# Optimization experiments

Measured on AMD Instinct MI355X. Metric: run time of the kernel, lower is better.

The kernel has to match this reference:

```python
import jax, jax.numpy as jnp
import numpy as np

N = 8192
IN, HID, NH, TOT = 64, 64, 4, 128
DH = TOT // NH  # 32


def setup_inputs() -> dict:
    key = jax.random.key(0)
    ks = jax.random.split(key, 8)
    s = 0.05
    return {
        "input": jax.random.normal(ks[0], (N, IN), jnp.float32),
        "hx": jax.random.normal(ks[1], (N, HID), jnp.float32),
        "Wq": jax.random.normal(ks[2], (NH, TOT, DH), jnp.float32) * s,
        "Wk": jax.random.normal(ks[3], (NH, TOT, DH), jnp.float32) * s,
        "Wr": jax.random.normal(ks[4], (TOT, HID), jnp.float32) * s,
        "br": jnp.zeros((HID,), jnp.float32),
        "Wz": jax.random.normal(ks[5], (TOT, HID), jnp.float32) * s,
        "bz": jnp.zeros((HID,), jnp.float32),
        "Wh": jax.random.normal(ks[6], (TOT, HID), jnp.float32) * s,
        "bh": jnp.zeros((HID,), jnp.float32),
    }


def _dyn_adj(x, Wq, Wk):
    # x: [N, T]; multi-head attention adjacency, averaged over heads -> [N, N]
    q = jnp.einsum('nt,htd->hnd', x, Wq)
    k = jnp.einsum('nt,htd->hnd', x, Wk)
    scores = jnp.einsum('hnd,hmd->hnm', q, k) / jnp.sqrt(jnp.float32(DH))
    return jnp.mean(jax.nn.softmax(scores, axis=-1), axis=0)  # [N, N]


def reference(input, hx, Wq, Wk, Wr, br, Wz, bz, Wh, bh):
    x = jnp.concatenate([input, hx], axis=1)          # [N, TOT]
    adj = _dyn_adj(x, Wq, Wk)                         # [N, N] row-stochastic
    ax = adj @ x                                      # shared adjacency application
    r = jax.nn.sigmoid(ax @ Wr + br)                  # [N, HID]
    z = jax.nn.sigmoid(ax @ Wz + bz)                  # [N, HID]
    x2 = jnp.concatenate([input, r * hx], axis=1)     # [N, TOT]
    h = jnp.tanh((adj @ x2) @ Wh + bh)                # [N, HID]
    return z * hx + (1.0 - z) * h
```

## Files before the change

kernel.cpp:

```cpp
#include <hip/hip_runtime.h>
#include <hip/hip_bf16.h>

#define NN 8192
#define TOTD 128
#define HIDD 64
#define NHEAD 4
#define DHD 32
#define NCQ 16
#define JPB (NN / 32 / NCQ)

typedef __attribute__((ext_vector_type(8))) short short8;
typedef __attribute__((ext_vector_type(4))) float f32x4;

__device__ __forceinline__ short f2b(float f) {
  unsigned u = __builtin_bit_cast(unsigned, f);
  u += 0x7fff + ((u >> 16) & 1);
  return (short)(u >> 16);
}
__device__ __forceinline__ short f2b_fast(float f) {
  unsigned u = __builtin_bit_cast(unsigned, f);
  return (short)((u + 0x8000u) >> 16);
}
__device__ __forceinline__ float fexp2(float x) {
#if __has_builtin(__builtin_amdgcn_exp2f)
  return __builtin_amdgcn_exp2f(x);
#else
  return exp2f(x);
#endif
}

__device__ __forceinline__ void gl_lds16(const short* g, short* l) {
  __builtin_amdgcn_global_load_lds(
      (const __attribute__((address_space(1))) void*)g,
      (__attribute__((address_space(3))) void*)l, 16, 0, 0);
}

__global__ void k_build_xfrag(const float* __restrict__ in, const float* __restrict__ hx,
                              short* __restrict__ xb) {
  int i = blockIdx.x * 256 + threadIdx.x;
  int n = i >> 7;
  int t = i & 127;
  float v = (t < 64) ? in[n * 64 + t] : hx[n * 64 + (t - 64)];
  int jt = n >> 5, kk = n & 31, cg = t >> 4;
  int l = ((kk >> 3) << 4) | (t & 15);
  xb[(((size_t)jt * 8 + cg) << 9) + (l << 3) + (kk & 7)] = f2b(v);
}

__global__ void k_qk(const float* __restrict__ in, const float* __restrict__ hx,
                     const float* __restrict__ Wq, const float* __restrict__ Wk,
                     short* __restrict__ qb, short* __restrict__ kb) {
  __shared__ float xr[TOTD];
  int n = blockIdx.x;
  int tid = threadIdx.x;
  if (tid < TOTD) xr[tid] = (tid < 64) ? in[n * 64 + tid] : hx[n * 64 + (tid - 64)];
  __syncthreads();
  int which = tid >> 7;
  int h = (tid >> 5) & 3;
  int d = tid & 31;
  const float* W = (which ? Wk : Wq) + h * TOTD * DHD + d;
  float acc = 0.f;
#pragma unroll
  for (int t = 0; t < TOTD; ++t) acc += xr[t] * W[t * DHD];
  int l = ((d >> 3) << 4) | (n & 15);
  if (!which) {
    acc *= 0.25503486f;
    qb[(((size_t)(n >> 4) * 4 + h) << 9) + (l << 3) + (d & 7)] = f2b(acc);
  } else {
    kb[((((size_t)(n >> 5) * 4 + h) * 2 + ((n >> 4) & 1)) << 9) + (l << 3) + (d & 7)] = f2b(acc);
  }
}

__global__ __launch_bounds__(256, 8) void k_denom(
    const short* __restrict__ qb, const short* __restrict__ kb,
    float* __restrict__ lpart_g) {
  __shared__ short kbuf[8 * 512];
  const int tid = threadIdx.x;
  const int w = tid >> 6, l = tid & 63;
  const int row16 = l & 15, grp = l >> 4;
  const int r0 = blockIdx.x * 64 + w * 16;
  const int rtile = blockIdx.x * 4 + w;
  const int jt0 = blockIdx.y * JPB;
  const f32x4 zero4 = {0.f, 0.f, 0.f, 0.f};

  short8 qf[NHEAD];
#pragma unroll
  for (int h = 0; h < NHEAD; ++h)
    qf[h] = *(const short8*)&qb[(((size_t)rtile * 4 + h) << 9) + l * 8];

  float acc[NHEAD][4];
#pragma unroll
  for (int h = 0; h < NHEAD; ++h)
#pragma unroll
    for (int r = 0; r < 4; ++r) acc[h][r] = 0.f;

  for (int j = 0; j < JPB; ++j) {
    int jt = jt0 + j;
#pragma unroll
    for (int c = w * 2; c < w * 2 + 2; ++c)
      gl_lds16(kb + (((size_t)jt * 8 + c) << 9) + l * 8, &kbuf[c * 512]);
    __syncthreads();
#pragma unroll
    for (int hs = 0; hs < 8; ++hs) {
      short8 kf = *(const short8*)&kbuf[hs * 512 + l * 8];
      f32x4 s = __builtin_amdgcn_mfma_f32_16x16x32_bf16(qf[hs >> 1], kf, zero4, 0, 0, 0);
#pragma unroll
      for (int r = 0; r < 4; ++r) acc[hs >> 1][r] += fexp2(s[r]);
    }
    __syncthreads();
  }
#pragma unroll
  for (int m = 1; m < 16; m <<= 1)
#pragma unroll
    for (int h = 0; h < NHEAD; ++h)
#pragma unroll
      for (int r = 0; r < 4; ++r) acc[h][r] += __shfl_xor(acc[h][r], m, 64);

  if (row16 == 0) {
#pragma unroll
    for (int h = 0; h < NHEAD; ++h)
#pragma unroll
      for (int r = 0; r < 4; ++r)
        lpart_g[((size_t)blockIdx.y * NHEAD + h) * NN + r0 + grp * 4 + r] = acc[h][r];
  }
}

__global__ void k_linv(const float* __restrict__ lpart_g, float* __restrict__ linv_g) {
  int i = blockIdx.x * 256 + threadIdx.x;
  float s = 0.f;
#pragma unroll
  for (int q = 0; q < NCQ; ++q) s += lpart_g[(size_t)q * NHEAD * NN + i];
  linv_g[i] = 0.25f / s;
}

__global__ __launch_bounds__(256, 5) void k_pv1(
    const short* __restrict__ qb, const short* __restrict__ kb,
    const short* __restrict__ xb, const float* __restrict__ linv_g,
    float* __restrict__ axq) {
  __shared__ short kxbuf[16 * 512];
  __shared__ short Plds[4][16][40];
  const int tid = threadIdx.x;
  const int w = tid >> 6, l = tid & 63;
  const int row16 = l & 15, grp = l >> 4;
  const int r0 = blockIdx.x * 64 + w * 16;
  const int rtile = blockIdx.x * 4 + w;
  const int jt0 = blockIdx.y * JPB;
  const f32x4 zero4 = {0.f, 0.f, 0.f, 0.f};

  short8 qf[NHEAD];
#pragma unroll
  for (int h = 0; h < NHEAD; ++h)
    qf[h] = *(const short8*)&qb[(((size_t)rtile * 4 + h) << 9) + l * 8];
  float linv[NHEAD][4];
#pragma unroll
  for (int h = 0; h < NHEAD; ++h)
#pragma unroll
    for (int r = 0; r < 4; ++r) linv[h][r] = linv_g[h * NN + r0 + grp * 4 + r];

  f32x4 axa[8];
#pragma unroll
  for (int cg = 0; cg < 8; ++cg) axa[cg] = zero4;

  for (int j = 0; j < JPB; ++j) {
    int jt = jt0 + j;
#pragma unroll
    for (int c = w * 4; c < w * 4 + 4; ++c) {
      const short* src = (c < 8) ? kb + (((size_t)jt * 8 + c) << 9) + l * 8
                                 : xb + (((size_t)jt * 8 + (c - 8)) << 9) + l * 8;
      gl_lds16(src, &kxbuf[c * 512]);
    }
    __syncthreads();
#pragma unroll
    for (int sub = 0; sub < 2; ++sub) {
      float p[4] = {0.f, 0.f, 0.f, 0.f};
#pragma unroll
      for (int h = 0; h < NHEAD; ++h) {
        short8 kf = *(const short8*)&kxbuf[(h * 2 + sub) * 512 + l * 8];
        f32x4 s = __builtin_amdgcn_mfma_f32_16x16x32_bf16(qf[h], kf, zero4, 0, 0, 0);
#pragma unroll
        for (int r = 0; r < 4; ++r) p[r] += fexp2(s[r]) * linv[h][r];
      }
#pragma unroll
      for (int r = 0; r < 4; ++r)
        Plds[w][grp * 4 + r][sub * 16 + row16] = f2b_fast(p[r]);
    }
    short8 pa = *(short8*)&Plds[w][row16][grp * 8];
#pragma unroll
    for (int cg = 0; cg < 8; ++cg) {
      short8 xv = *(const short8*)&kxbuf[(8 + cg) * 512 + l * 8];
      axa[cg] = __builtin_amdgcn_mfma_f32_16x16x32_bf16(pa, xv, axa[cg], 0, 0, 0);
    }
    __syncthreads();
  }
#pragma unroll
  for (int cg = 0; cg < 8; ++cg)
#pragma unroll
    for (int r = 0; r < 4; ++r)
      axq[(size_t)blockIdx.y * NN * TOTD + (size_t)(r0 + grp * 4 + r) * TOTD + cg * 16 + row16] =
          axa[cg][r];
}

__global__ void k_rz(const float* __restrict__ axq, const float* __restrict__ hx,
                     const float* __restrict__ Wr, const float* __restrict__ br,
                     const float* __restrict__ Wz, const float* __restrict__ bz,
                     float* __restrict__ ax, float* __restrict__ z,
                     short* __restrict__ v2f) {
  __shared__ float axs[2][TOTD];
  int tid = threadIdx.x;
  int rr = tid >> 7;
  int c2 = tid & 127;
  int n = blockIdx.x * 2 + rr;
  float s = 0.f;
#pragma unroll
  for (int q = 0; q < NCQ; ++q) s += axq[(size_t)q * NN * TOTD + (size_t)n * TOTD + c2];
  axs[rr][c2] = s;
  ax[(size_t)n * TOTD + c2] = s;
  __syncthreads();
  bool isz = c2 >= HIDD;
  int c = c2 & (HIDD - 1);
  const float* W = isz ? Wz : Wr;
  float acc = isz ? bz[c] : br[c];
#pragma unroll
  for (int t = 0; t < TOTD; ++t) acc += axs[rr][t] * W[t * HIDD + c];
  float sg = 1.f / (1.f + __expf(-acc));
  if (isz) {
    z[n * HIDD + c] = sg;
  } else {
    int jt = n >> 5, kk = n & 31, cg = c >> 4;
    int ll = ((kk >> 3) << 4) | (c & 15);
    v2f[(((size_t)jt * 4 + cg) << 9) + (ll << 3) + (kk & 7)] = f2b(sg * hx[n * HIDD + c]);
  }
}

__global__ __launch_bounds__(256, 5) void k_pv2(
    const short* __restrict__ qb, const short* __restrict__ kb,
    const short* __restrict__ v2f, const float* __restrict__ linv_g,
    float* __restrict__ a2q) {
  __shared__ short kvbuf[12 * 512];
  __shared__ short Plds[4][16][40];
  const int tid = threadIdx.x;
  const int w = tid >> 6, l = tid & 63;
  const int row16 = l & 15, grp = l >> 4;
  const int r0 = blockIdx.x * 64 + w * 16;
  const int rtile = blockIdx.x * 4 + w;
  const int jt0 = blockIdx.y * JPB;
  const f32x4 zero4 = {0.f, 0.f, 0.f, 0.f};

  short8 qf[NHEAD];
#pragma unroll
  for (int h = 0; h < NHEAD; ++h)
    qf[h] = *(const short8*)&qb[(((size_t)rtile * 4 + h) << 9) + l * 8];
  float linv[NHEAD][4];
#pragma unroll
  for (int h = 0; h < NHEAD; ++h)
#pragma unroll
    for (int r = 0; r < 4; ++r) linv[h][r] = linv_g[h * NN + r0 + grp * 4 + r];

  f32x4 a2a[4];
#pragma unroll
  for (int cg = 0; cg < 4; ++cg) a2a[cg] = zero4;

  for (int j = 0; j < JPB; ++j) {
    int jt = jt0 + j;
#pragma unroll
    for (int c = w * 3; c < w * 3 + 3; ++c) {
      const short* src = (c < 8) ? kb + (((size_t)jt * 8 + c) << 9) + l * 8
                                 : v2f + (((size_t)jt * 4 + (c - 8)) << 9) + l * 8;
      gl_lds16(src, &kvbuf[c * 512]);
    }
    __syncthreads();
#pragma unroll
    for (int sub = 0; sub < 2; ++sub) {
      float p[4] = {0.f, 0.f, 0.f, 0.f};
#pragma unroll
      for (int h = 0; h < NHEAD; ++h) {
        short8 kf = *(const short8*)&kvbuf[(h * 2 + sub) * 512 + l * 8];
        f32x4 s = __builtin_amdgcn_mfma_f32_16x16x32_bf16(qf[h], kf, zero4, 0, 0, 0);
#pragma unroll
        for (int r = 0; r < 4; ++r) p[r] += fexp2(s[r]) * linv[h][r];
      }
#pragma unroll
      for (int r = 0; r < 4; ++r)
        Plds[w][grp * 4 + r][sub * 16 + row16] = f2b_fast(p[r]);
    }
    short8 pa = *(short8*)&Plds[w][row16][grp * 8];
#pragma unroll
    for (int cg = 0; cg < 4; ++cg) {
      short8 vv = *(const short8*)&kvbuf[(8 + cg) * 512 + l * 8];
      a2a[cg] = __builtin_amdgcn_mfma_f32_16x16x32_bf16(pa, vv, a2a[cg], 0, 0, 0);
    }
    __syncthreads();
  }
#pragma unroll
  for (int cg = 0; cg < 4; ++cg)
#pragma unroll
    for (int r = 0; r < 4; ++r)
      a2q[(size_t)blockIdx.y * NN * HIDD + (size_t)(r0 + grp * 4 + r) * HIDD + cg * 16 + row16] =
          a2a[cg][r];
}

__global__ __launch_bounds__(256) void k_final(
    const float* __restrict__ a2q, const float* __restrict__ ax,
    const float* __restrict__ hx, const float* __restrict__ Wh,
    const float* __restrict__ bh, const float* __restrict__ z,
    float* __restrict__ out) {
  __shared__ float Whs[TOTD * HIDD];
  __shared__ float a2s[16][HIDD];
  const int tid = threadIdx.x;
  const int r0 = blockIdx.x * 16;

  for (int i = tid; i < TOTD * HIDD; i += 256) Whs[i] = Wh[i];
  for (int i = tid; i < 16 * HIDD; i += 256) {
    int rw = i >> 6, c = i & 63;
    size_t gi = (size_t)(r0 + rw) * HIDD + c;
    float s = 0.f;
#pragma unroll
    for (int q = 0; q < NCQ; ++q) s += a2q[(size_t)q * NN * HIDD + gi];
    a2s[rw][c] = s;
  }
  __syncthreads();
  for (int o = tid; o < 16 * HIDD; o += 256) {
    int rw = o >> 6, c = o & 63;
    const float* axrow = &ax[(size_t)(r0 + rw) * TOTD];
    float acc = bh[c];
#pragma unroll
    for (int t = 0; t < 64; ++t) acc += axrow[t] * Whs[t * HIDD + c];
#pragma unroll
    for (int t = 0; t < 64; ++t) acc += a2s[rw][t] * Whs[(64 + t) * HIDD + c];
    float hval = tanhf(acc);
    size_t gi = (size_t)(r0 + rw) * HIDD + c;
    float zz = z[gi];
    out[gi] = zz * hx[gi] + (1.f - zz) * hval;
  }
}

extern "C" void kernel_launch(void* const* d_in, const int* in_sizes, int n_in,
                              void* d_out, int out_size, void* d_ws, size_t ws_size,
                              hipStream_t stream) {
  const float* in = (const float*)d_in[0];
  const float* hx = (const float*)d_in[1];
  const float* Wq = (const float*)d_in[2];
  const float* Wk = (const float*)d_in[3];
  const float* Wr = (const float*)d_in[4];
  const float* br = (const float*)d_in[5];
  const float* Wz = (const float*)d_in[6];
  const float* bz = (const float*)d_in[7];
  const float* Wh = (const float*)d_in[8];
  const float* bh = (const float*)d_in[9];

  const size_t MB = 1ull << 20;
  char* ws = (char*)d_ws;
  short* qb    = (short*)(ws + 0 * MB);
  short* kb    = (short*)(ws + 2 * MB);
  short* xb    = (short*)(ws + 4 * MB);
  float* linv  = (float*)(ws + 6 * MB);
  float* lpart = (float*)(ws + 7 * MB);
  float* ax    = (float*)(ws + 10 * MB);
  float* z     = (float*)(ws + 14 * MB);
  short* v2f   = (short*)(ws + 16 * MB);
  float* axq   = (float*)(ws + 20 * MB);
  float* a2q   = (float*)(ws + 84 * MB);
  float* out   = (float*)d_out;

  k_build_xfrag<<<dim3((NN * TOTD) / 256), dim3(256), 0, stream>>>(in, hx, xb);
  k_qk<<<dim3(NN), dim3(256), 0, stream>>>(in, hx, Wq, Wk, qb, kb);
  k_denom<<<dim3(NN / 64, NCQ), dim3(256), 0, stream>>>(qb, kb, lpart);
  k_linv<<<dim3((NHEAD * NN) / 256), dim3(256), 0, stream>>>(lpart, linv);
  k_pv1<<<dim3(NN / 64, NCQ), dim3(256), 0, stream>>>(qb, kb, xb, linv, axq);
  k_rz<<<dim3(NN / 2), dim3(256), 0, stream>>>(axq, hx, Wr, br, Wz, bz, ax, z, v2f);
  k_pv2<<<dim3(NN / 64, NCQ), dim3(256), 0, stream>>>(qb, kb, v2f, linv, a2q);
  k_final<<<dim3(NN / 16), dim3(256), 0, stream>>>(a2q, ax, hx, Wh, bh, z, out);
}
```

Measured before the change: 239.1 us.

## Load K and X fragments directly from global into registers, drop LDS staging

Replaces the cooperative global-to-LDS staging of K and X/V tiles in the denominator and PV kernels with per-wave direct global loads into registers. This removes both __syncthreads per iteration and the LDS round trip. The cost is that each of the four waves now fetches the same K/X tiles separately, relying on L1/L2 to absorb the redundant traffic. Register pressure also rises, so the PV kernels' launch-bounds occupancy hint drops from 5 to 4.

```diff
diff --git a/kernel.cpp b/kernel.cpp
--- a/kernel.cpp
+++ b/kernel.cpp
@@ -27,12 +27,6 @@
 #else
   return exp2f(x);
 #endif
-}
-
-__device__ __forceinline__ void gl_lds16(const short* g, short* l) {
-  __builtin_amdgcn_global_load_lds(
-      (const __attribute__((address_space(1))) void*)g,
-      (__attribute__((address_space(3))) void*)l, 16, 0, 0);
 }
 
 __global__ void k_build_xfrag(const float* __restrict__ in, const float* __restrict__ hx,
@@ -73,7 +67,6 @@
 __global__ __launch_bounds__(256, 8) void k_denom(
     const short* __restrict__ qb, const short* __restrict__ kb,
     float* __restrict__ lpart_g) {
-  __shared__ short kbuf[8 * 512];
   const int tid = threadIdx.x;
   const int w = tid >> 6, l = tid & 63;
   const int row16 = l & 15, grp = l >> 4;
@@ -94,19 +87,14 @@
     for (int r = 0; r < 4; ++r) acc[h][r] = 0.f;
 
   for (int j = 0; j < JPB; ++j) {
-    int jt = jt0 + j;
-#pragma unroll
-    for (int c = w * 2; c < w * 2 + 2; ++c)
-      gl_lds16(kb + (((size_t)jt * 8 + c) << 9) + l * 8, &kbuf[c * 512]);
-    __syncthreads();
+    const short* kbase = kb + (((size_t)(jt0 + j) * 8) << 9) + l * 8;
 #pragma unroll
     for (int hs = 0; hs < 8; ++hs) {
-      short8 kf = *(const short8*)&kbuf[hs * 512 + l * 8];
+      short8 kf = *(const short8*)&kbase[hs << 9];
       f32x4 s = __builtin_amdgcn_mfma_f32_16x16x32_bf16(qf[hs >> 1], kf, zero4, 0, 0, 0);
 #pragma unroll
       for (int r = 0; r < 4; ++r) acc[hs >> 1][r] += fexp2(s[r]);
     }
-    __syncthreads();
   }
 #pragma unroll
   for (int m = 1; m < 16; m <<= 1)
@@ -132,11 +120,10 @@
   linv_g[i] = 0.25f / s;
 }
 
-__global__ __launch_bounds__(256, 5) void k_pv1(
+__global__ __launch_bounds__(256, 4) void k_pv1(
     const short* __restrict__ qb, const short* __restrict__ kb,
     const short* __restrict__ xb, const float* __restrict__ linv_g,
     float* __restrict__ axq) {
-  __shared__ short kxbuf[16 * 512];
   __shared__ short Plds[4][16][40];
   const int tid = threadIdx.x;
   const int w = tid >> 6, l = tid & 63;
@@ -161,20 +148,23 @@
   for (int cg = 0; cg < 8; ++cg) axa[cg] = zero4;
 
   for (int j = 0; j < JPB; ++j) {
-    int jt = jt0 + j;
-#pragma unroll
-    for (int c = w * 4; c < w * 4 + 4; ++c) {
-      const short* src = (c < 8) ? kb + (((size_t)jt * 8 + c) << 9) + l * 8
-                                 : xb + (((size_t)jt * 8 + (c - 8)) << 9) + l * 8;
-      gl_lds16(src, &kxbuf[c * 512]);
-    }
-    __syncthreads();
+    const size_t jt = jt0 + j;
+    const short* kbase = kb + ((jt * 8) << 9) + l * 8;
+    const short* xbase = xb + ((jt * 8) << 9) + l * 8;
+    short8 xv0 = *(const short8*)&xbase[0 << 9];
+    short8 xv1 = *(const short8*)&xbase[1 << 9];
+    short8 xv2 = *(const short8*)&xbase[2 << 9];
+    short8 xv3 = *(const short8*)&xbase[3 << 9];
+    short8 xv4 = *(const short8*)&xbase[4 << 9];
+    short8 xv5 = *(const short8*)&xbase[5 << 9];
+    short8 xv6 = *(const short8*)&xbase[6 << 9];
+    short8 xv7 = *(const short8*)&xbase[7 << 9];
 #pragma unroll
     for (int sub = 0; sub < 2; ++sub) {
       float p[4] = {0.f, 0.f, 0.f, 0.f};
 #pragma unroll
       for (int h = 0; h < NHEAD; ++h) {
-        short8 kf = *(const short8*)&kxbuf[(h * 2 + sub) * 512 + l * 8];
+        short8 kf = *(const short8*)&kbase[(h * 2 + sub) << 9];
         f32x4 s = __builtin_amdgcn_mfma_f32_16x16x32_bf16(qf[h], kf, zero4, 0, 0, 0);
 #pragma unroll
         for (int r = 0; r < 4; ++r) p[r] += fexp2(s[r]) * linv[h][r];
@@ -184,12 +174,14 @@
         Plds[w][grp * 4 + r][sub * 16 + row16] = f2b_fast(p[r]);
     }
     short8 pa = *(short8*)&Plds[w][row16][grp * 8];
-#pragma unroll
-    for (int cg = 0; cg < 8; ++cg) {
-      short8 xv = *(const short8*)&kxbuf[(8 + cg) * 512 + l * 8];
-      axa[cg] = __builtin_amdgcn_mfma_f32_16x16x32_bf16(pa, xv, axa[cg], 0, 0, 0);
-    }
-    __syncthreads();
+    axa[0] = __builtin_amdgcn_mfma_f32_16x16x32_bf16(pa, xv0, axa[0], 0, 0, 0);
+    axa[1] = __builtin_amdgcn_mfma_f32_16x16x32_bf16(pa, xv1, axa[1], 0, 0, 0);
+    axa[2] = __builtin_amdgcn_mfma_f32_16x16x32_bf16(pa, xv2, axa[2], 0, 0, 0);
+    axa[3] = __builtin_amdgcn_mfma_f32_16x16x32_bf16(pa, xv3, axa[3], 0, 0, 0);
+    axa[4] = __builtin_amdgcn_mfma_f32_16x16x32_bf16(pa, xv4, axa[4], 0, 0, 0);
+    axa[5] = __builtin_amdgcn_mfma_f32_16x16x32_bf16(pa, xv5, axa[5], 0, 0, 0);
+    axa[6] = __builtin_amdgcn_mfma_f32_16x16x32_bf16(pa, xv6, axa[6], 0, 0, 0);
+    axa[7] = __builtin_amdgcn_mfma_f32_16x16x32_bf16(pa, xv7, axa[7], 0, 0, 0);
   }
 #pragma unroll
   for (int cg = 0; cg < 8; ++cg)
@@ -231,11 +223,10 @@
   }
 }
 
-__global__ __launch_bounds__(256, 5) void k_pv2(
+__global__ __launch_bounds__(256, 4) void k_pv2(
     const short* __restrict__ qb, const short* __restrict__ kb,
     const short* __restrict__ v2f, const float* __restrict__ linv_g,
     float* __restrict__ a2q) {
-  __shared__ short kvbuf[12 * 512];
   __shared__ short Plds[4][16][40];
   const int tid = threadIdx.x;
   const int w = tid >> 6, l = tid & 63;
@@ -260,20 +251,19 @@
   for (int cg = 0; cg < 4; ++cg) a2a[cg] = zero4;
 
   for (int j = 0; j < JPB; ++j) {
-    int jt = jt0 + j;
-#pragma unroll
-    for (int c = w * 3; c < w * 3 + 3; ++c) {
-      const short* src = (c < 8) ? kb + (((size_t)jt * 8 + c) << 9) + l * 8
-                                 : v2f + (((size_t)jt * 4 + (c - 8)) << 9) + l * 8;
-      gl_lds16(src, &kvbuf[c * 512]);
-    }
-    __syncthreads();
+    const size_t jt = jt0 + j;
+    const short* kbase = kb + ((jt * 8) << 9) + l * 8;
+    const short* vbase = v2f + ((jt * 4) << 9) + l * 8;
+    short8 vv0 = *(const short8*)&vbase[0 << 9];
+    short8 vv1 = *(const short8*)&vbase[1 << 9];
+    short8 vv2 = *(const short8*)&vbase[2 << 9];
+    short8 vv3 = *(const short8*)&vbase[3 << 9];
 #pragma unroll
     for (int sub = 0; sub < 2; ++sub) {
       float p[4] = {0.f, 0.f, 0.f, 0.f};
 #pragma unroll
       for (int h = 0; h < NHEAD; ++h) {
-        short8 kf = *(const short8*)&kvbuf[(h * 2 + sub) * 512 + l * 8];
+        short8 kf = *(const short8*)&kbase[(h * 2 + sub) << 9];
         f32x4 s = __builtin_amdgcn_mfma_f32_16x16x32_bf16(qf[h], kf, zero4, 0, 0, 0);
 #pragma unroll
         for (int r = 0; r < 4; ++r) p[r] += fexp2(s[r]) * linv[h][r];
@@ -283,12 +273,10 @@
         Plds[w][grp * 4 + r][sub * 16 + row16] = f2b_fast(p[r]);
     }
     short8 pa = *(short8*)&Plds[w][row16][grp * 8];
-#pragma unroll
-    for (int cg = 0; cg < 4; ++cg) {
-      short8 vv = *(const short8*)&kvbuf[(8 + cg) * 512 + l * 8];
-      a2a[cg] = __builtin_amdgcn_mfma_f32_16x16x32_bf16(pa, vv, a2a[cg], 0, 0, 0);
-    }
-    __syncthreads();
+    a2a[0] = __builtin_amdgcn_mfma_f32_16x16x32_bf16(pa, vv0, a2a[0], 0, 0, 0);
+    a2a[1] = __builtin_amdgcn_mfma_f32_16x16x32_bf16(pa, vv1, a2a[1], 0, 0, 0);
+    a2a[2] = __builtin_amdgcn_mfma_f32_16x16x32_bf16(pa, vv2, a2a[2], 0, 0, 0);
+    a2a[3] = __builtin_amdgcn_mfma_f32_16x16x32_bf16(pa, vv3, a2a[3], 0, 0, 0);
   }
 #pragma unroll
   for (int cg = 0; cg < 4; ++cg)
```

After: 256.0 us. 7.1% more time.
